# Performance work log

Hardware: AMD Instinct MI355X
Metric: run time of the kernel (lower is better)

## Reference

```python
import jax, jax.numpy as jnp
import numpy as np

N, H, M, B = 64, 64, 32, 16384
relu = jax.nn.relu


def setup_inputs() -> dict:
    key = jax.random.key(0)
    ks = jax.random.split(key, 10)
    s = 0.05
    x = jax.random.normal(ks[0], (B, N), dtype=jnp.float32)
    # stacked per-node weights (torch Linear applies x @ W.T, W: [out, in])
    W1a = jax.random.normal(ks[1], (N, H, N), dtype=jnp.float32) * s   # directed net layer 1
    W1b = jax.random.normal(ks[2], (N, M, H), dtype=jnp.float32) * s   # directed net layer 2
    W2a = jax.random.normal(ks[3], (N, H, N), dtype=jnp.float32) * s   # bi-directed net layer 1
    W2b = jax.random.normal(ks[4], (N, M, H), dtype=jnp.float32) * s   # bi-directed net layer 2
    W3a = jax.random.normal(ks[5], (N, H, 2 * M + N), dtype=jnp.float32) * s  # fuse layer 1
    b3a = jax.random.normal(ks[6], (N, H), dtype=jnp.float32) * s
    W3b = jax.random.normal(ks[7], (N, 1, H), dtype=jnp.float32) * s          # fuse layer 2
    b3b = jax.random.normal(ks[8], (N, 1), dtype=jnp.float32) * s
    return {"x": x, "W1a": W1a, "W1b": W1b, "W2a": W2a, "W2b": W2b,
            "W3a": W3a, "b3a": b3a, "W3b": W3b, "b3b": b3b}


def reference(x, W1a, W1b, W2a, W2b, W3a, b3a, W3b, b3b):
    Bsz, n = x.shape
    eye = jnp.eye(n, dtype=x.dtype)
    off = 1.0 - eye  # filter_1; adjacency at init is also (ones - eye), so mask is idempotent
    # inputs_1_dag / inputs_1_bi: [B, N, N] per-node masked copies of x
    x1 = jnp.einsum('bn,in->bin', x, off)
    # inputs_2: [B, N, N] with x[b,i] on the diagonal of row i
    x2 = eye[None, :, :] * x[:, None, :]
    # directed branch: ReLU(Linear) -> ReLU(Linear), batched over node i
    r1 = relu(jnp.einsum('bih,imh->bim', relu(jnp.einsum('bin,ihn->bih', x1, W1a)), W1b))
    # bi-directed branch (same masked input at init)
    r2 = relu(jnp.einsum('bih,imh->bim', relu(jnp.einsum('bin,ihn->bih', x1, W2a)), W2b))
    feat = jnp.concatenate([r1, r2, x2], axis=2)  # [B, N, 2M+N]
    h = relu(jnp.einsum('bik,ihk->bih', feat, W3a) + b3a[None])
    out = relu(jnp.einsum('bih,ioh->bio', h, W3b) + b3b[None])  # [B, N, 1]
    return out[..., 0]  # [B, N] causal derivative
```

## Files before the change

### kernel.cpp

```cpp
#include <hip/hip_runtime.h>


typedef short bf16x8 __attribute__((ext_vector_type(8)));
typedef float f32x4  __attribute__((ext_vector_type(4)));
typedef unsigned int u32x4 __attribute__((ext_vector_type(4)));

__device__ __forceinline__ unsigned int pack2(float a, float b) {
    unsigned int r;
    asm("v_cvt_pk_bf16_f32 %0, %1, %2" : "=v"(r) : "v"(a), "v"(b));
    return r;
}

__device__ __forceinline__ f32x4 mfma16(bf16x8 a, bf16x8 b, f32x4 c) {
    return __builtin_amdgcn_mfma_f32_16x16x32_bf16(a, b, c, 0, 0, 0);
}

__device__ __forceinline__ bf16x8 ds_read_pin(unsigned byte_off) {
    bf16x8 r;
    asm volatile("ds_read_b128 %0, %1\n\ts_waitcnt lgkmcnt(0)"
                 : "=v"(r) : "v"(byte_off));
    return r;
}
__device__ __forceinline__ f32x4 ds_read_pin_f(unsigned byte_off) {
    f32x4 r;
    asm volatile("ds_read_b128 %0, %1\n\ts_waitcnt lgkmcnt(0)"
                 : "=v"(r) : "v"(byte_off));
    return r;
}

__device__ __forceinline__ bf16x8 pack_frag(f32x4 lo, f32x4 hi) {
    union { u32x4 u; bf16x8 v; } r;
    r.u[0] = pack2(fmaxf(lo[0], 0.f), fmaxf(lo[1], 0.f));
    r.u[1] = pack2(fmaxf(lo[2], 0.f), fmaxf(lo[3], 0.f));
    r.u[2] = pack2(fmaxf(hi[0], 0.f), fmaxf(hi[1], 0.f));
    r.u[3] = pack2(fmaxf(hi[2], 0.f), fmaxf(hi[3], 0.f));
    return r.v;
}

__device__ __forceinline__ bf16x8 cvt_frag2(const float* __restrict__ plo,
                                            const float* __restrict__ phi) {
    f32x4 f0 = *(const f32x4*)plo;
    f32x4 f1 = *(const f32x4*)phi;
    union { u32x4 u; bf16x8 v; } r;
    r.u[0] = pack2(f0[0], f0[1]);
    r.u[1] = pack2(f0[2], f0[3]);
    r.u[2] = pack2(f1[0], f1[1]);
    r.u[3] = pack2(f1[2], f1[3]);
    return r.v;
}

__device__ __forceinline__ bf16x8 cvt_frag2_m(const float* __restrict__ plo,
                                              const float* __restrict__ phi,
                                              const unsigned int* M) {
    f32x4 f0 = *(const f32x4*)plo;
    f32x4 f1 = *(const f32x4*)phi;
    union { u32x4 u; bf16x8 v; } r;
    r.u[0] = pack2(f0[0], f0[1]) & M[0];
    r.u[1] = pack2(f0[2], f0[3]) & M[1];
    r.u[2] = pack2(f1[0], f1[1]) & M[2];
    r.u[3] = pack2(f1[2], f1[3]) & M[3];
    return r.v;
}

__global__ __launch_bounds__(256) void prep_x(const float* __restrict__ x,
                                              unsigned short* __restrict__ xb) {
    int j = (blockIdx.x * 256 + threadIdx.x) * 8;
    f32x4 a = *(const f32x4*)&x[j];
    f32x4 b = *(const f32x4*)&x[j + 4];
    u32x4 r = { pack2(a[0], a[1]), pack2(a[2], a[3]), pack2(b[0], b[1]), pack2(b[2], b[3]) };
    *(u32x4*)&xb[j] = r;
}

__global__ __launch_bounds__(256, 2) void main_kernel(
    const float* __restrict__ x,
    const float* __restrict__ W1a, const float* __restrict__ W1b,
    const float* __restrict__ W2a, const float* __restrict__ W2b,
    const float* __restrict__ W3a, const float* __restrict__ b3a,
    const float* __restrict__ W3b, const float* __restrict__ b3b,
    const unsigned short* __restrict__ xb,
    float* __restrict__ out)
{
    const int i    = blockIdx.x & 63;
    const int bg   = blockIdx.x >> 6;
    const int tid  = threadIdx.x;
    const int w    = tid >> 6;
    const int lane = tid & 63;
    const int q    = lane >> 4;
    const int c0   = lane & 15;

    __shared__ short lds[28160];

    unsigned int M[2][4];
    {
        const unsigned int halfmask = (i & 1) ? 0x0000FFFFu : 0xFFFF0000u;
        const int dz = (i >> 1) & 3;
        #pragma unroll
        for (int s = 0; s < 2; ++s) {
            bool hit = ((i >> 3) == s * 4 + q);
            #pragma unroll
            for (int d = 0; d < 4; ++d)
                M[s][d] = (hit && d == dz) ? halfmask : 0xFFFFFFFFu;
        }
    }

    if (w == 0) {
        const float* p1 = W1a + (i << 12);
        #pragma unroll
        for (int j = 0; j < 8; ++j) {
            int t = j >> 1, s = j & 1;
            int off = (((t << 4) + c0) << 6) + (s << 5) + (q << 3);
            bf16x8 fr = cvt_frag2_m(p1 + off, p1 + off + 4, M[s]);
            *(bf16x8*)&lds[j * 512 + lane * 8] = fr;
        }
    } else if (w == 1) {
        const float* p2 = W2a + (i << 12);
        #pragma unroll
        for (int j = 0; j < 8; ++j) {
            int t = j >> 1, s = j & 1;
            int off = (((t << 4) + c0) << 6) + (s << 5) + (q << 3);
            bf16x8 fr = cvt_frag2_m(p2 + off, p2 + off + 4, M[s]);
            *(bf16x8*)&lds[(8 + j) * 512 + lane * 8] = fr;
        }
    } else if (w == 2) {
        const float* p3 = W3a + (i << 13);
        #pragma unroll
        for (int j = 0; j < 8; ++j) {
            int t = j >> 1, s = j & 1;
            int base = (((t << 4) + c0) << 7) + (s << 5) + (q << 2);
            bf16x8 fr = cvt_frag2(p3 + base, p3 + base + 16);
            *(bf16x8*)&lds[(16 + j) * 512 + lane * 8] = fr;
        }
    } else {
        const float* pb1 = W1b + (i << 11);
        const float* pb2 = W2b + (i << 11);
        #pragma unroll
        for (int j = 0; j < 4; ++j) {
            int t = j >> 1, s = j & 1;
            int base = (((t << 4) + c0) << 6) + (s << 5) + (q << 2);
            bf16x8 fr1 = cvt_frag2(pb1 + base, pb1 + base + 16);
            bf16x8 fr2 = cvt_frag2(pb2 + base, pb2 + base + 16);
            *(bf16x8*)&lds[(24 + j) * 512 + lane * 8] = fr1;
            *(bf16x8*)&lds[(28 + j) * 512 + lane * 8] = fr2;
        }
    }
    if (tid < 64) {
        float* sv = (float*)&lds[16384];
        int tt = tid >> 4, qq = (tid >> 2) & 3, rr = tid & 3;
        sv[0 * 64 + tt * 16 + qq * 4 + rr] = b3a[(i << 6) + tid];
        sv[2 * 64 + tt * 16 + qq * 4 + rr] = W3b[(i << 6) + tid];
        sv[1 * 64 + tt * 16 + qq * 4 + rr] = W3a[(i << 13) + (tid << 7) + 64 + i];
    }
    const float bb = b3b[i];
    __syncthreads();

    const unsigned lbase = (unsigned)(lane * 16);
    bf16x8 A1f[4][2], A2f[4][2];
    #pragma unroll
    for (int t = 0; t < 4; ++t)
        #pragma unroll
        for (int s = 0; s < 2; ++s) {
            A1f[t][s] = ds_read_pin((unsigned)((t * 2 + s) * 1024) + lbase);
            A2f[t][s] = ds_read_pin((unsigned)((8 + t * 2 + s) * 1024) + lbase);
        }
    const unsigned vbase = 32768u + (unsigned)(q << 4);
    f32x4 b3av[4], w3xv[4], w3bv[4];
    #pragma unroll
    for (int t = 0; t < 4; ++t) {
        b3av[t] = ds_read_pin_f(vbase + 0u * 256u + (unsigned)(t << 6));
        w3xv[t] = ds_read_pin_f(vbase + 1u * 256u + (unsigned)(t << 6));
        w3bv[t] = ds_read_pin_f(vbase + 2u * 256u + (unsigned)(t << 6));
    }

    const int wbase = (((bg << 2) + w) << 9);

    bf16x8 XB0[2], XB1[2]; float xd[2];
    #pragma unroll
    for (int r = 0; r < 2; ++r) {
        int rw = wbase + (r << 4) + c0;
        XB0[r] = *(const bf16x8*)&xb[(rw << 6) + (q << 3)];
        XB1[r] = *(const bf16x8*)&xb[(rw << 6) + 32 + (q << 3)];
        xd[r]  = x[(rw << 6) + i];
    }

    for (int k = 0; k < 16; ++k) {
        int nb = wbase + ((k < 15 ? k + 1 : 15) << 5) + c0;
        bf16x8 nXB0[2], nXB1[2]; float nxd[2];
        #pragma unroll
        for (int r = 0; r < 2; ++r) {
            int rw = nb + (r << 4);
            nXB0[r] = *(const bf16x8*)&xb[(rw << 6) + (q << 3)];
            nXB1[r] = *(const bf16x8*)&xb[(rw << 6) + 32 + (q << 3)];
            nxd[r]  = x[(rw << 6) + i];
        }

        f32x4 a1[4][2], a2[4][2];
        #pragma unroll
        for (int t = 0; t < 4; ++t) {
            #pragma unroll
            for (int r = 0; r < 2; ++r) {
                f32x4 z = {0.f, 0.f, 0.f, 0.f};
                a1[t][r] = mfma16(A1f[t][1], XB1[r], mfma16(A1f[t][0], XB0[r], z));
                a2[t][r] = mfma16(A2f[t][1], XB1[r], mfma16(A2f[t][0], XB0[r], z));
            }
        }
        bf16x8 HB0[2], HB1[2], GB0[2], GB1[2];
        #pragma unroll
        for (int r = 0; r < 2; ++r) {
            HB0[r] = pack_frag(a1[0][r], a1[1][r]);
            HB1[r] = pack_frag(a1[2][r], a1[3][r]);
            GB0[r] = pack_frag(a2[0][r], a2[1][r]);
            GB1[r] = pack_frag(a2[2][r], a2[3][r]);
        }

        f32x4 b1[2][2], b2[2][2];
        #pragma unroll
        for (int t = 0; t < 2; ++t) {
            bf16x8 g10 = *(const bf16x8*)&lds[(24 + t * 2 + 0) * 512 + lane * 8];
            bf16x8 g11 = *(const bf16x8*)&lds[(24 + t * 2 + 1) * 512 + lane * 8];
            bf16x8 g20 = *(const bf16x8*)&lds[(28 + t * 2 + 0) * 512 + lane * 8];
            bf16x8 g21 = *(const bf16x8*)&lds[(28 + t * 2 + 1) * 512 + lane * 8];
            #pragma unroll
            for (int r = 0; r < 2; ++r) {
                f32x4 z = {0.f, 0.f, 0.f, 0.f};
                b1[t][r] = mfma16(g11, HB1[r], mfma16(g10, HB0[r], z));
                b2[t][r] = mfma16(g21, GB1[r], mfma16(g20, GB0[r], z));
            }
        }
        bf16x8 RB0[2], RB1[2];
        #pragma unroll
        for (int r = 0; r < 2; ++r) {
            RB0[r] = pack_frag(b1[0][r], b1[1][r]);
            RB1[r] = pack_frag(b2[0][r], b2[1][r]);
        }

        float p[2] = {0.f, 0.f};
        #pragma unroll
        for (int t = 0; t < 4; ++t) {
            bf16x8 h0 = *(const bf16x8*)&lds[(16 + t * 2 + 0) * 512 + lane * 8];
            bf16x8 h1 = *(const bf16x8*)&lds[(16 + t * 2 + 1) * 512 + lane * 8];
            #pragma unroll
            for (int r = 0; r < 2; ++r) {
                f32x4 acc;
                #pragma unroll
                for (int e = 0; e < 4; ++e) acc[e] = fmaf(xd[r], w3xv[t][e], b3av[t][e]);
                acc = mfma16(h0, RB0[r], acc);
                acc = mfma16(h1, RB1[r], acc);
                #pragma unroll
                for (int e = 0; e < 4; ++e) p[r] = fmaf(fmaxf(acc[e], 0.f), w3bv[t][e], p[r]);
            }
        }
        #pragma unroll
        for (int r = 0; r < 2; ++r) {
            float pp = p[r];
            pp += __shfl_xor(pp, 16);
            pp += __shfl_xor(pp, 32);
            int rw = wbase + (k << 5) + (r << 4) + c0;
            if (lane < 16) out[(rw << 6) + i] = fmaxf(pp + bb, 0.f);
        }

        #pragma unroll
        for (int r = 0; r < 2; ++r) { XB0[r] = nXB0[r]; XB1[r] = nXB1[r]; xd[r] = nxd[r]; }
    }
}

extern "C" void kernel_launch(void* const* d_in, const int* in_sizes, int n_in,
                              void* d_out, int out_size, void* d_ws, size_t ws_size,
                              hipStream_t stream) {
    (void)in_sizes; (void)n_in; (void)out_size; (void)ws_size;
    const float* x   = (const float*)d_in[0];
    const float* W1a = (const float*)d_in[1];
    const float* W1b = (const float*)d_in[2];
    const float* W2a = (const float*)d_in[3];
    const float* W2b = (const float*)d_in[4];
    const float* W3a = (const float*)d_in[5];
    const float* b3a = (const float*)d_in[6];
    const float* W3b = (const float*)d_in[7];
    const float* b3b = (const float*)d_in[8];
    float* out = (float*)d_out;
    unsigned short* xb = (unsigned short*)d_ws;

    prep_x<<<512, 256, 0, stream>>>(x, xb);
    main_kernel<<<512, 256, 0, stream>>>(x, W1a, W1b, W2a, W2b, W3a, b3a, W3b, b3b, xb, out);
}
```

Before: 117.5 us.

## Reload layer-1 weights from LDS per tile and widen batch tile to 64 rows

Measured after the change: 114.7 us (median of 2 runs). -2.4%, faster.

```diff
diff --git a/kernel.cpp b/kernel.cpp
--- a/kernel.cpp
+++ b/kernel.cpp
@@ -13,19 +13,6 @@
 
 __device__ __forceinline__ f32x4 mfma16(bf16x8 a, bf16x8 b, f32x4 c) {
     return __builtin_amdgcn_mfma_f32_16x16x32_bf16(a, b, c, 0, 0, 0);
-}
-
-__device__ __forceinline__ bf16x8 ds_read_pin(unsigned byte_off) {
-    bf16x8 r;
-    asm volatile("ds_read_b128 %0, %1\n\ts_waitcnt lgkmcnt(0)"
-                 : "=v"(r) : "v"(byte_off));
-    return r;
-}
-__device__ __forceinline__ f32x4 ds_read_pin_f(unsigned byte_off) {
-    f32x4 r;
-    asm volatile("ds_read_b128 %0, %1\n\ts_waitcnt lgkmcnt(0)"
-                 : "=v"(r) : "v"(byte_off));
-    return r;
 }
 
 __device__ __forceinline__ bf16x8 pack_frag(f32x4 lo, f32x4 hi) {
@@ -153,66 +140,46 @@
     const float bb = b3b[i];
     __syncthreads();
 
-    const unsigned lbase = (unsigned)(lane * 16);
-    bf16x8 A1f[4][2], A2f[4][2];
-    #pragma unroll
-    for (int t = 0; t < 4; ++t)
-        #pragma unroll
-        for (int s = 0; s < 2; ++s) {
-            A1f[t][s] = ds_read_pin((unsigned)((t * 2 + s) * 1024) + lbase);
-            A2f[t][s] = ds_read_pin((unsigned)((8 + t * 2 + s) * 1024) + lbase);
-        }
-    const unsigned vbase = 32768u + (unsigned)(q << 4);
-    f32x4 b3av[4], w3xv[4], w3bv[4];
-    #pragma unroll
-    for (int t = 0; t < 4; ++t) {
-        b3av[t] = ds_read_pin_f(vbase + 0u * 256u + (unsigned)(t << 6));
-        w3xv[t] = ds_read_pin_f(vbase + 1u * 256u + (unsigned)(t << 6));
-        w3bv[t] = ds_read_pin_f(vbase + 2u * 256u + (unsigned)(t << 6));
-    }
+    const float* sv = (const float*)&lds[16384];
 
     const int wbase = (((bg << 2) + w) << 9);
 
-    bf16x8 XB0[2], XB1[2]; float xd[2];
-    #pragma unroll
-    for (int r = 0; r < 2; ++r) {
-        int rw = wbase + (r << 4) + c0;
-        XB0[r] = *(const bf16x8*)&xb[(rw << 6) + (q << 3)];
-        XB1[r] = *(const bf16x8*)&xb[(rw << 6) + 32 + (q << 3)];
-        xd[r]  = x[(rw << 6) + i];
-    }
-
-    for (int k = 0; k < 16; ++k) {
-        int nb = wbase + ((k < 15 ? k + 1 : 15) << 5) + c0;
-        bf16x8 nXB0[2], nXB1[2]; float nxd[2];
-        #pragma unroll
-        for (int r = 0; r < 2; ++r) {
-            int rw = nb + (r << 4);
-            nXB0[r] = *(const bf16x8*)&xb[(rw << 6) + (q << 3)];
-            nXB1[r] = *(const bf16x8*)&xb[(rw << 6) + 32 + (q << 3)];
-            nxd[r]  = x[(rw << 6) + i];
-        }
-
-        f32x4 a1[4][2], a2[4][2];
+    for (int k = 0; k < 8; ++k) {
+        const int cb = wbase + (k << 6) + c0;
+
+        bf16x8 XB0[4], XB1[4]; float xd[4];
+        #pragma unroll
+        for (int r = 0; r < 4; ++r) {
+            int rw = cb + (r << 4);
+            XB0[r] = *(const bf16x8*)&xb[(rw << 6) + (q << 3)];
+            XB1[r] = *(const bf16x8*)&xb[(rw << 6) + 32 + (q << 3)];
+            xd[r]  = x[(rw << 6) + i];
+        }
+
+        f32x4 a1[4][4], a2[4][4];
         #pragma unroll
         for (int t = 0; t < 4; ++t) {
-            #pragma unroll
-            for (int r = 0; r < 2; ++r) {
+            bf16x8 f10 = *(const bf16x8*)&lds[(t * 2 + 0) * 512 + lane * 8];
+            bf16x8 f11 = *(const bf16x8*)&lds[(t * 2 + 1) * 512 + lane * 8];
+            bf16x8 f20 = *(const bf16x8*)&lds[(8 + t * 2 + 0) * 512 + lane * 8];
+            bf16x8 f21 = *(const bf16x8*)&lds[(8 + t * 2 + 1) * 512 + lane * 8];
+            #pragma unroll
+            for (int r = 0; r < 4; ++r) {
                 f32x4 z = {0.f, 0.f, 0.f, 0.f};
-                a1[t][r] = mfma16(A1f[t][1], XB1[r], mfma16(A1f[t][0], XB0[r], z));
-                a2[t][r] = mfma16(A2f[t][1], XB1[r], mfma16(A2f[t][0], XB0[r], z));
+                a1[t][r] = mfma16(f11, XB1[r], mfma16(f10, XB0[r], z));
+                a2[t][r] = mfma16(f21, XB1[r], mfma16(f20, XB0[r], z));
             }
         }
-        bf16x8 HB0[2], HB1[2], GB0[2], GB1[2];
-        #pragma unroll
-        for (int r = 0; r < 2; ++r) {
+        bf16x8 HB0[4], HB1[4], GB0[4], GB1[4];
+        #pragma unroll
+        for (int r = 0; r < 4; ++r) {
             HB0[r] = pack_frag(a1[0][r], a1[1][r]);
             HB1[r] = pack_frag(a1[2][r], a1[3][r]);
             GB0[r] = pack_frag(a2[0][r], a2[1][r]);
             GB1[r] = pack_frag(a2[2][r], a2[3][r]);
         }
 
-        f32x4 b1[2][2], b2[2][2];
+        f32x4 b1[2][4], b2[2][4];
         #pragma unroll
         for (int t = 0; t < 2; ++t) {
             bf16x8 g10 = *(const bf16x8*)&lds[(24 + t * 2 + 0) * 512 + lane * 8];
@@ -220,46 +187,46 @@
             bf16x8 g20 = *(const bf16x8*)&lds[(28 + t * 2 + 0) * 512 + lane * 8];
             bf16x8 g21 = *(const bf16x8*)&lds[(28 + t * 2 + 1) * 512 + lane * 8];
             #pragma unroll
-            for (int r = 0; r < 2; ++r) {
+            for (int r = 0; r < 4; ++r) {
                 f32x4 z = {0.f, 0.f, 0.f, 0.f};
                 b1[t][r] = mfma16(g11, HB1[r], mfma16(g10, HB0[r], z));
                 b2[t][r] = mfma16(g21, GB1[r], mfma16(g20, GB0[r], z));
             }
         }
-        bf16x8 RB0[2], RB1[2];
-        #pragma unroll
-        for (int r = 0; r < 2; ++r) {
+        bf16x8 RB0[4], RB1[4];
+        #pragma unroll
+        for (int r = 0; r < 4; ++r) {
             RB0[r] = pack_frag(b1[0][r], b1[1][r]);
             RB1[r] = pack_frag(b2[0][r], b2[1][r]);
         }
 
-        float p[2] = {0.f, 0.f};
+        float p[4] = {0.f, 0.f, 0.f, 0.f};
         #pragma unroll
         for (int t = 0; t < 4; ++t) {
             bf16x8 h0 = *(const bf16x8*)&lds[(16 + t * 2 + 0) * 512 + lane * 8];
             bf16x8 h1 = *(const bf16x8*)&lds[(16 + t * 2 + 1) * 512 + lane * 8];
-            #pragma unroll
-            for (int r = 0; r < 2; ++r) {
+            f32x4 bv = *(const f32x4*)&sv[0 * 64 + t * 16 + q * 4];
+            f32x4 xv = *(const f32x4*)&sv[1 * 64 + t * 16 + q * 4];
+            f32x4 wv = *(const f32x4*)&sv[2 * 64 + t * 16 + q * 4];
+            #pragma unroll
+            for (int r = 0; r < 4; ++r) {
                 f32x4 acc;
                 #pragma unroll
-                for (int e = 0; e < 4; ++e) acc[e] = fmaf(xd[r], w3xv[t][e], b3av[t][e]);
+                for (int e = 0; e < 4; ++e) acc[e] = fmaf(xd[r], xv[e], bv[e]);
                 acc = mfma16(h0, RB0[r], acc);
                 acc = mfma16(h1, RB1[r], acc);
                 #pragma unroll
-                for (int e = 0; e < 4; ++e) p[r] = fmaf(fmaxf(acc[e], 0.f), w3bv[t][e], p[r]);
+                for (int e = 0; e < 4; ++e) p[r] = fmaf(fmaxf(acc[e], 0.f), wv[e], p[r]);
             }
         }
         #pragma unroll
-        for (int r = 0; r < 2; ++r) {
+        for (int r = 0; r < 4; ++r) {
             float pp = p[r];
             pp += __shfl_xor(pp, 16);
             pp += __shfl_xor(pp, 32);
-            int rw = wbase + (k << 5) + (r << 4) + c0;
+            int rw = cb + (r << 4);
             if (lane < 16) out[(rw << 6) + i] = fmaxf(pp + bb, 0.f);
         }
-
-        #pragma unroll
-        for (int r = 0; r < 2; ++r) { XB0[r] = nXB0[r]; XB1[r] = nXB1[r]; xd[r] = nxd[r]; }
     }
 }
 
```
